# Optimization experiments

Hardware: AMD Instinct MI355X
Metric: run time of the kernel (lower is better)

The kernel has to match this reference:

```python
import jax, jax.numpy as jnp
import numpy as np

DMODEL = 1024
NHEAD = 16
HDIM = DMODEL // NHEAD
CTXLEN = 2048
BATCH = 2


def setup_inputs() -> dict:
    key = jax.random.key(0)
    k_x, k_qkv, k_pw, k_pb = jax.random.split(key, 4)
    x = jax.random.normal(k_x, (BATCH, CTXLEN, DMODEL), dtype=jnp.float32)
    # nn.Linear weights: stored as [out, in]; init scale ~ 1/sqrt(in)
    s = 1.0 / np.sqrt(DMODEL)
    w_qkv = jax.random.uniform(k_qkv, (3 * DMODEL, DMODEL), minval=-s, maxval=s, dtype=jnp.float32)
    w_proj = jax.random.uniform(k_pw, (DMODEL, DMODEL), minval=-s, maxval=s, dtype=jnp.float32)
    b_proj = jax.random.uniform(k_pb, (DMODEL,), minval=-s, maxval=s, dtype=jnp.float32)
    return {"x": x, "w_qkv": w_qkv, "w_proj": w_proj, "b_proj": b_proj}


def reference(x, w_qkv, w_proj, b_proj):
    b, t, c = x.shape
    qkv = jnp.einsum('btc,oc->bto', x, w_qkv)  # [b, t, 3c]
    q, k, v = jnp.split(qkv, 3, axis=-1)
    # [b, nhead, t, hdim]
    q = q.reshape(b, t, NHEAD, HDIM).transpose(0, 2, 1, 3)
    k = k.reshape(b, t, NHEAD, HDIM).transpose(0, 2, 1, 3)
    v = v.reshape(b, t, NHEAD, HDIM).transpose(0, 2, 1, 3)
    # NOTE: original code MULTIPLIES by sqrt(hdim) (not the usual divide)
    att = jnp.einsum('bhqd,bhkd->bhqk', q, k) * (HDIM ** 0.5)
    causal = jnp.tril(jnp.ones((t, t), dtype=bool))  # [t, t]
    att = jnp.where(causal[None, None], att, -jnp.inf)
    att = jax.nn.softmax(att, axis=-1)
    y = jnp.einsum('bhqk,bhkd->bhqd', att, v)
    y = y.transpose(0, 2, 1, 3).reshape(b, t, c)
    return jnp.einsum('btc,oc->bto', y, w_proj) + b_proj
```

## Files before the change

### kernel.cpp

```cpp
#include <hip/hip_runtime.h>
#include <hip/hip_bf16.h>

#define DMODEL 1024
#define NHEAD 16
#define HDIM 64
#define CTXLEN 2048
#define BATCH 2
#define M_TOTAL (BATCH * CTXLEN)

typedef unsigned short ushort_t;
typedef __attribute__((ext_vector_type(8))) _Float16 f16x8;
typedef __attribute__((ext_vector_type(8))) unsigned short u16x8;
typedef __attribute__((ext_vector_type(4))) float f32x4;
typedef __attribute__((ext_vector_type(4))) unsigned short u16x4;

__device__ __forceinline__ unsigned short f32_f16(float f) {
    return __builtin_bit_cast(unsigned short, (_Float16)f);
}
__device__ __forceinline__ float fast_exp2(float x) {
    return __builtin_amdgcn_exp2f(x);
}
__device__ __forceinline__ f32x4 mfma16f(f16x8 a, f16x8 b, f32x4 c) {
    return __builtin_amdgcn_mfma_f32_16x16x32_f16(a, b, c, 0, 0, 0);
}
__device__ __forceinline__ void gload_lds16(const ushort_t* g, ushort_t* l) {
    __builtin_amdgcn_global_load_lds(
        (const __attribute__((address_space(1))) void*)g,
        (__attribute__((address_space(3))) void*)l, 16, 0, 0);
}

__global__ __launch_bounds__(256)
void conv_f32_f16(const float* __restrict__ src, ushort_t* __restrict__ dst, int n4) {
    for (int i = blockIdx.x * blockDim.x + threadIdx.x; i < n4;
         i += gridDim.x * blockDim.x) {
        const float4 v = reinterpret_cast<const float4*>(src)[i];
        u16x4 o;
        o[0] = f32_f16(v.x); o[1] = f32_f16(v.y);
        o[2] = f32_f16(v.z); o[3] = f32_f16(v.w);
        reinterpret_cast<u16x4*>(dst)[i] = o;
    }
}

template<bool QKV_EPI>
__global__ __launch_bounds__(256)
void gemm_f16_nt(const ushort_t* __restrict__ A, const ushort_t* __restrict__ B,
                 const float* __restrict__ bias, float* __restrict__ C,
                 ushort_t* __restrict__ qf, ushort_t* __restrict__ kf,
                 ushort_t* __restrict__ vb,
                 int M, int N, int K) {
    __shared__ ushort_t lds[2 * 4096];

    const int tid  = threadIdx.x;
    const int lane = tid & 63;
    const int wave = tid >> 6;
    const int lc   = lane & 15;
    const int lg   = lane >> 4;
    const int wr   = wave >> 1;
    const int wc   = wave & 1;
    const int row0 = blockIdx.y * 128;
    const int col0 = blockIdx.x * 128;

    const int c0 = tid, c1 = 256 + tid;
    const int r0 = c0 >> 2, l0 = (c0 & 3) ^ ((c0 >> 3) & 3);
    const int r1 = c1 >> 2, l1 = (c1 & 3) ^ ((c1 >> 3) & 3);
    const size_t gaoff0 = (size_t)(row0 + r0) * K + l0 * 8;
    const size_t gaoff1 = (size_t)(row0 + r1) * K + l1 * 8;
    const size_t gboff0 = (size_t)(col0 + r0) * K + l0 * 8;
    const size_t gboff1 = (size_t)(col0 + r1) * K + l1 * 8;
    const int ld0 = c0 * 8, ld1 = c1 * 8;

    int aoff[4], boff[4];
    #pragma unroll
    for (int m = 0; m < 4; ++m) {
        const int ra = wr * 64 + m * 16 + lc;
        aoff[m] = ra * 32 + ((lg ^ ((ra >> 1) & 3)) * 8);
        const int rb = wc * 64 + m * 16 + lc;
        boff[m] = rb * 32 + ((lg ^ ((rb >> 1) & 3)) * 8);
    }

    f32x4 acc[4][4];
    const f32x4 zero4 = {0.f, 0.f, 0.f, 0.f};
    #pragma unroll
    for (int m = 0; m < 4; ++m)
        #pragma unroll
        for (int n = 0; n < 4; ++n) acc[m][n] = zero4;

    const int NT = K >> 5;

    auto stage = [&](int kt) {
        const int ko = kt * 32;
        gload_lds16(A + gaoff0 + ko, &lds[ld0]);
        gload_lds16(A + gaoff1 + ko, &lds[ld1]);
        gload_lds16(B + gboff0 + ko, &lds[4096 + ld0]);
        gload_lds16(B + gboff1 + ko, &lds[4096 + ld1]);
    };

    stage(0);
    for (int kt = 0; kt < NT; ++kt) {
        __syncthreads();
        f16x8 fa[4], fb[4];
        #pragma unroll
        for (int m = 0; m < 4; ++m) {
            fa[m] = *reinterpret_cast<const f16x8*>(&lds[aoff[m]]);
            fb[m] = *reinterpret_cast<const f16x8*>(&lds[4096 + boff[m]]);
        }
        __syncthreads();
        if (kt + 1 < NT) stage(kt + 1);
        #pragma unroll
        for (int m = 0; m < 4; ++m)
            #pragma unroll
            for (int n = 0; n < 4; ++n)
                acc[m][n] = mfma16f(fa[m], fb[n], acc[m][n]);
    }

    if (!QKV_EPI) {
        #pragma unroll
        for (int m = 0; m < 4; ++m)
            #pragma unroll
            for (int i = 0; i < 4; ++i) {
                const int r = row0 + wr * 64 + m * 16 + lg * 4 + i;
                #pragma unroll
                for (int n = 0; n < 4; ++n) {
                    const int c = col0 + wc * 64 + n * 16 + lc;
                    C[(size_t)r * N + c] = acc[m][n][i] + bias[c];
                }
            }
    } else {
        #pragma unroll
        for (int m = 0; m < 4; ++m)
            #pragma unroll
            for (int i = 0; i < 4; ++i) {
                const int r = row0 + wr * 64 + m * 16 + lg * 4 + i;
                const int bb = r >> 11;
                const int t  = r & 2047;
                #pragma unroll
                for (int n = 0; n < 4; ++n) {
                    const int cg  = col0 + wc * 64 + n * 16 + lc;
                    const int sec = cg >> 10;
                    const int ch  = cg & 1023;
                    const int hh  = ch >> 6;
                    const int d   = ch & 63;
                    const size_t off = (((size_t)(bb * NHEAD + hh)) * CTXLEN + t) * HDIM + d;
                    const unsigned short hv = f32_f16(acc[m][n][i]);
                    if (sec == 0)      qf[off] = hv;
                    else if (sec == 1) kf[off] = hv;
                    else               vb[off] = hv;
                }
            }
    }
}

__global__ __launch_bounds__(256)
void transpose_v(const ushort_t* __restrict__ vb, ushort_t* __restrict__ vt) {
    __shared__ ushort_t T[64][66];
    const int tt = blockIdx.x;
    const int bh = blockIdx.y;
    const int tid = threadIdx.x;
    const int r  = tid >> 2;
    const int c0 = (tid & 3) * 16;

    const ushort_t* src = vb + ((size_t)bh * CTXLEN + tt * 64) * HDIM;
    #pragma unroll
    for (int half = 0; half < 2; ++half) {
        const u16x8 v = *reinterpret_cast<const u16x8*>(&src[(size_t)r * HDIM + c0 + half * 8]);
        #pragma unroll
        for (int j = 0; j < 8; ++j) T[r][c0 + half * 8 + j] = v[j];
    }
    __syncthreads();
    ushort_t* dst = vt + ((size_t)bh * HDIM + r) * CTXLEN + tt * 64 + c0;
    u16x8 o0, o1;
    #pragma unroll
    for (int j = 0; j < 8; ++j) { o0[j] = T[c0 + j][r]; o1[j] = T[c0 + 8 + j][r]; }
    *reinterpret_cast<u16x8*>(&dst[0]) = o0;
    *reinterpret_cast<u16x8*>(&dst[8]) = o1;
}

#define SCALE_LOG2 11.5415603271f

__global__ __launch_bounds__(256)
void attn_fwd6(const ushort_t* __restrict__ qf, const ushort_t* __restrict__ kf,
               const ushort_t* __restrict__ vt, ushort_t* __restrict__ yb) {
    __shared__ ushort_t KH[2][4096];
    __shared__ ushort_t VT[2][4096];
    __shared__ ushort_t Ps[4][16][64];

    const int id   = blockIdx.x;
    const int bh   = id & 31;
    const int qraw = id >> 5;
    const int jj   = qraw >> 3, g = qraw & 7;
    const int qb   = 8 * jj + ((jj & 1) ? g : 7 - g);
    const int b    = bh >> 4;
    const int h    = bh & 15;

    const int tid  = threadIdx.x;
    const int wave = tid >> 6;
    const int lane = tid & 63;
    const int lc   = lane & 15;
    const int lg   = lane >> 4;

    const ushort_t* kfb = kf + (size_t)bh * CTXLEN * HDIM;
    const ushort_t* vtb = vt + (size_t)bh * HDIM * CTXLEN;

    const int cA = tid, cB = 256 + tid;
    const int rA = cA >> 3, sgA = (cA & 7) ^ (rA & 7);
    const int rB = cB >> 3, sgB = (cB & 7) ^ (rB & 7);

    auto stage = [&](int kb, int buf) {
        const size_t koff = (size_t)(kb * 64);
        gload_lds16(kfb + (koff + rA) * HDIM + sgA * 8, &KH[buf][cA * 8]);
        gload_lds16(kfb + (koff + rB) * HDIM + sgB * 8, &KH[buf][cB * 8]);
        gload_lds16(vtb + (size_t)rA * CTXLEN + kb * 64 + sgA * 8, &VT[buf][cA * 8]);
        gload_lds16(vtb + (size_t)rB * CTXLEN + kb * 64 + sgB * 8, &VT[buf][cB * 8]);
    };

    const size_t qrow = (size_t)bh * CTXLEN + qb * 64 + wave * 16 + lc;
    f16x8 qfr[2];
    #pragma unroll
    for (int ds = 0; ds < 2; ++ds)
        qfr[ds] = *reinterpret_cast<const f16x8*>(&qf[qrow * HDIM + ds * 32 + lg * 8]);

    const f32x4 zero4 = {0.f, 0.f, 0.f, 0.f};
    f32x4 yacc[4];
    #pragma unroll
    for (int t = 0; t < 4; ++t) yacc[t] = zero4;
    float m_i = -1e30f, l_i = 0.f;

    stage(0, 0);
    __syncthreads();

    int cur = 0;
    for (int kb = 0; kb <= qb; ++kb) {
        if (kb < qb) stage(kb + 1, cur ^ 1);

        f16x8 kfr[4][2];
        #pragma unroll
        for (int tc = 0; tc < 4; ++tc) {
            const int rk = tc * 16 + lc;
            #pragma unroll
            for (int ds = 0; ds < 2; ++ds) {
                const int a = rk * 64 + (((ds * 4 + lg) ^ (rk & 7)) * 8);
                kfr[tc][ds] = *reinterpret_cast<const f16x8*>(&KH[cur][a]);
            }
        }
        f16x8 vf[4][2];
        #pragma unroll
        for (int t = 0; t < 4; ++t) {
            const int rv = t * 16 + lc;
            #pragma unroll
            for (int ks = 0; ks < 2; ++ks) {
                const int a = rv * 64 + (((ks * 4 + lg) ^ (rv & 7)) * 8);
                vf[t][ks] = *reinterpret_cast<const f16x8*>(&VT[cur][a]);
            }
        }

        f32x4 sacc[4];
        #pragma unroll
        for (int tc = 0; tc < 4; ++tc) sacc[tc] = zero4;
        __builtin_amdgcn_s_setprio(1);
        #pragma unroll
        for (int tc = 0; tc < 4; ++tc)
            #pragma unroll
            for (int ds = 0; ds < 2; ++ds)
                sacc[tc] = mfma16f(kfr[tc][ds], qfr[ds], sacc[tc]);
        __builtin_amdgcn_s_setprio(0);

        const bool diag = (kb == qb);
        const int q_loc = wave * 16 + lc;
        float p[4][4];
        #pragma unroll
        for (int tc = 0; tc < 4; ++tc)
            #pragma unroll
            for (int i = 0; i < 4; ++i) {
                float u = sacc[tc][i] * SCALE_LOG2;
                if (diag && (tc * 16 + lg * 4 + i) > q_loc) u = -1e30f;
                p[tc][i] = u;
            }
        float mx = p[0][0];
        #pragma unroll
        for (int tc = 0; tc < 4; ++tc)
            #pragma unroll
            for (int i = 0; i < 4; ++i) mx = fmaxf(mx, p[tc][i]);
        mx = fmaxf(mx, __shfl_xor(mx, 16));
        mx = fmaxf(mx, __shfl_xor(mx, 32));
        const float mnew = fmaxf(m_i, mx);
        const float corr = fast_exp2(m_i - mnew);
        float psum = 0.f;
        #pragma unroll
        for (int tc = 0; tc < 4; ++tc)
            #pragma unroll
            for (int i = 0; i < 4; ++i) {
                const float e = fast_exp2(p[tc][i] - mnew);
                p[tc][i] = e;
                psum += e;
            }
        psum += __shfl_xor(psum, 16);
        psum += __shfl_xor(psum, 32);
        l_i = l_i * corr + psum;
        m_i = mnew;
        #pragma unroll
        for (int t = 0; t < 4; ++t) yacc[t] *= corr;

        #pragma unroll
        for (int tc = 0; tc < 4; ++tc) {
            const int eb = tc * 16 + lg * 4;
            const int se = ((((eb >> 3) ^ (lc & 7)) << 3) | (eb & 7));
            u16x4 pk;
            #pragma unroll
            for (int i = 0; i < 4; ++i) pk[i] = f32_f16(p[tc][i]);
            *reinterpret_cast<u16x4*>(&Ps[wave][lc][se]) = pk;
        }
        f16x8 pa[2];
        #pragma unroll
        for (int ks = 0; ks < 2; ++ks) {
            const int sl = ((ks * 4 + lg) ^ (lc & 7)) << 3;
            pa[ks] = *reinterpret_cast<const f16x8*>(&Ps[wave][lc][sl]);
        }
        __builtin_amdgcn_s_setprio(1);
        #pragma unroll
        for (int t = 0; t < 4; ++t)
            #pragma unroll
            for (int ks = 0; ks < 2; ++ks)
                yacc[t] = mfma16f(vf[t][ks], pa[ks], yacc[t]);
        __builtin_amdgcn_s_setprio(0);

        __syncthreads();
        cur ^= 1;
    }

    const float inv = 1.0f / l_i;
    ushort_t* base = yb + (size_t)(b * CTXLEN + qb * 64 + wave * 16 + lc) * DMODEL
                     + h * HDIM;
    #pragma unroll
    for (int t = 0; t < 4; ++t) {
        u16x4 o;
        #pragma unroll
        for (int i = 0; i < 4; ++i) o[i] = f32_f16(yacc[t][i] * inv);
        *reinterpret_cast<u16x4*>(&base[t * 16 + lg * 4]) = o;
    }
}

extern "C" void kernel_launch(void* const* d_in, const int* in_sizes, int n_in,
                              void* d_out, int out_size, void* d_ws, size_t ws_size,
                              hipStream_t stream) {
    const float* x      = (const float*)d_in[0];
    const float* w_qkv  = (const float*)d_in[1];
    const float* w_proj = (const float*)d_in[2];
    const float* b_proj = (const float*)d_in[3];
    float* out = (float*)d_out;

    char* ws = (char*)d_ws;
    ushort_t* wqf = (ushort_t*)(ws);
    ushort_t* wpf = (ushort_t*)(ws + 6291456);
    ushort_t* xf  = (ushort_t*)(ws + 8388608);
    ushort_t* qf  = (ushort_t*)(ws + 16777216);
    ushort_t* kf  = (ushort_t*)(ws + 25165824);
    ushort_t* vb  = (ushort_t*)(ws + 33554432);
    ushort_t* vt  = (ushort_t*)(ws + 41943040);
    ushort_t* yb  = xf;

    const dim3 blk(256);

    conv_f32_f16<<<dim3(2048), blk, 0, stream>>>(x, xf, M_TOTAL * DMODEL / 4);
    conv_f32_f16<<<dim3(2048), blk, 0, stream>>>(w_qkv, wqf, 3 * DMODEL * DMODEL / 4);
    conv_f32_f16<<<dim3(1024), blk, 0, stream>>>(w_proj, wpf, DMODEL * DMODEL / 4);

    gemm_f16_nt<true><<<dim3(3 * DMODEL / 128, M_TOTAL / 128), blk, 0, stream>>>(
        xf, wqf, nullptr, nullptr, qf, kf, vb, M_TOTAL, 3 * DMODEL, DMODEL);

    transpose_v<<<dim3(CTXLEN / 64, BATCH * NHEAD), blk, 0, stream>>>(vb, vt);

    attn_fwd6<<<dim3(1024), blk, 0, stream>>>(qf, kf, vt, yb);

    gemm_f16_nt<false><<<dim3(DMODEL / 128, M_TOTAL / 128), blk, 0, stream>>>(
        yb, wpf, b_proj, out, nullptr, nullptr, nullptr, M_TOTAL, DMODEL, DMODEL);
}
```

Measured before the change: 127.4 us.

## Split causal attention KV range into units with a separate merge kernel

Splits each query tile's key range into up to four units, with more units for later tiles, so the 2560 blocks do roughly equal work. Each unit writes its unnormalized partial output plus running max and sum to workspace, and a new merge kernel combines them with log-sum-exp weights before writing y. This targets load imbalance and the tail of long diagonal-heavy blocks in the causal attention. In exchange it adds an extra launch and extra global traffic for the partial results, and the partials are rounded to fp16 before normalization.

```diff
diff --git a/kernel.cpp b/kernel.cpp
--- a/kernel.cpp
+++ b/kernel.cpp
@@ -17,6 +17,9 @@
 __device__ __forceinline__ unsigned short f32_f16(float f) {
     return __builtin_bit_cast(unsigned short, (_Float16)f);
 }
+__device__ __forceinline__ float f16_f32(unsigned short h) {
+    return (float)__builtin_bit_cast(_Float16, h);
+}
 __device__ __forceinline__ float fast_exp2(float x) {
     return __builtin_amdgcn_exp2f(x);
 }
@@ -27,6 +30,12 @@
     __builtin_amdgcn_global_load_lds(
         (const __attribute__((address_space(1))) void*)g,
         (__attribute__((address_space(3))) void*)l, 16, 0, 0);
+}
+__device__ __forceinline__ int unit_off(int qt) {
+    if (qt < 8)  return qt;
+    if (qt < 16) return 8 + (qt - 8) * 2;
+    if (qt < 24) return 24 + (qt - 16) * 3;
+    return 48 + (qt - 24) * 4;
 }
 
 __global__ __launch_bounds__(256)
@@ -178,19 +187,27 @@
 #define SCALE_LOG2 11.5415603271f
 
 __global__ __launch_bounds__(256)
-void attn_fwd6(const ushort_t* __restrict__ qf, const ushort_t* __restrict__ kf,
-               const ushort_t* __restrict__ vt, ushort_t* __restrict__ yb) {
+void attn_fwd7(const ushort_t* __restrict__ qf, const ushort_t* __restrict__ kf,
+               const ushort_t* __restrict__ vt,
+               ushort_t* __restrict__ py, float* __restrict__ pml) {
     __shared__ ushort_t KH[2][4096];
     __shared__ ushort_t VT[2][4096];
     __shared__ ushort_t Ps[4][16][64];
 
-    const int id   = blockIdx.x;
-    const int bh   = id & 31;
-    const int qraw = id >> 5;
-    const int jj   = qraw >> 3, g = qraw & 7;
-    const int qb   = 8 * jj + ((jj & 1) ? g : 7 - g);
-    const int b    = bh >> 4;
-    const int h    = bh & 15;
+    const int id    = blockIdx.x;
+    const int bh    = id & 31;
+    const int u_off = id >> 5;
+    int qt, u;
+    if (u_off < 8)       { qt = u_off;                          u = 0; }
+    else if (u_off < 24) { const int t = u_off - 8;  qt = 8  + (t >> 1); u = t & 1; }
+    else if (u_off < 48) { const int t = u_off - 24; const int q3 = t / 3; qt = 16 + q3; u = t - q3 * 3; }
+    else                 { const int t = u_off - 48; qt = 24 + (t >> 2); u = t & 3; }
+    const int total = qt + 1;
+    const int nu    = (qt >> 3) + 1;
+    const int base  = total / nu, rem = total % nu;
+    const int kb0   = u * base + (u < rem ? u : rem);
+    const int len   = base + (u < rem ? 1 : 0);
+    const int slot  = bh * 80 + u_off;
 
     const int tid  = threadIdx.x;
     const int wave = tid >> 6;
@@ -213,7 +230,7 @@
         gload_lds16(vtb + (size_t)rB * CTXLEN + kb * 64 + sgB * 8, &VT[buf][cB * 8]);
     };
 
-    const size_t qrow = (size_t)bh * CTXLEN + qb * 64 + wave * 16 + lc;
+    const size_t qrow = (size_t)bh * CTXLEN + qt * 64 + wave * 16 + lc;
     f16x8 qfr[2];
     #pragma unroll
     for (int ds = 0; ds < 2; ++ds)
@@ -225,12 +242,13 @@
     for (int t = 0; t < 4; ++t) yacc[t] = zero4;
     float m_i = -1e30f, l_i = 0.f;
 
-    stage(0, 0);
+    stage(kb0, 0);
     __syncthreads();
 
     int cur = 0;
-    for (int kb = 0; kb <= qb; ++kb) {
-        if (kb < qb) stage(kb + 1, cur ^ 1);
+    for (int s = 0; s < len; ++s) {
+        const int kb = kb0 + s;
+        if (s + 1 < len) stage(kb + 1, cur ^ 1);
 
         f16x8 kfr[4][2];
         #pragma unroll
@@ -264,16 +282,16 @@
                 sacc[tc] = mfma16f(kfr[tc][ds], qfr[ds], sacc[tc]);
         __builtin_amdgcn_s_setprio(0);
 
-        const bool diag = (kb == qb);
+        const bool diag = (kb == qt);
         const int q_loc = wave * 16 + lc;
         float p[4][4];
         #pragma unroll
         for (int tc = 0; tc < 4; ++tc)
             #pragma unroll
             for (int i = 0; i < 4; ++i) {
-                float u = sacc[tc][i] * SCALE_LOG2;
-                if (diag && (tc * 16 + lg * 4 + i) > q_loc) u = -1e30f;
-                p[tc][i] = u;
+                float uu = sacc[tc][i] * SCALE_LOG2;
+                if (diag && (tc * 16 + lg * 4 + i) > q_loc) uu = -1e30f;
+                p[tc][i] = uu;
             }
         float mx = p[0][0];
         #pragma unroll
@@ -327,16 +345,79 @@
         cur ^= 1;
     }
 
-    const float inv = 1.0f / l_i;
-    ushort_t* base = yb + (size_t)(b * CTXLEN + qb * 64 + wave * 16 + lc) * DMODEL
-                     + h * HDIM;
+    const int row = wave * 16 + lc;
+    ushort_t* prow = py + ((size_t)slot * 64 + row) * 64;
     #pragma unroll
     for (int t = 0; t < 4; ++t) {
         u16x4 o;
         #pragma unroll
-        for (int i = 0; i < 4; ++i) o[i] = f32_f16(yacc[t][i] * inv);
-        *reinterpret_cast<u16x4*>(&base[t * 16 + lg * 4]) = o;
-    }
+        for (int i = 0; i < 4; ++i) o[i] = f32_f16(yacc[t][i]);
+        *reinterpret_cast<u16x4*>(&prow[t * 16 + lg * 4]) = o;
+    }
+    if (lg == 0) {
+        pml[(size_t)slot * 128 + row]      = m_i;
+        pml[(size_t)slot * 128 + 64 + row] = l_i;
+    }
+}
+
+__global__ __launch_bounds__(256)
+void merge_attn(const ushort_t* __restrict__ py, const float* __restrict__ pml,
+                ushort_t* __restrict__ yb) {
+    const int bid = blockIdx.x;
+    const int bh  = bid >> 5;
+    const int qt  = bid & 31;
+    const int b   = bh >> 4;
+    const int h   = bh & 15;
+    const int tid = threadIdx.x;
+    const int row = tid >> 2;
+    const int d0  = (tid & 3) * 16;
+
+    const int nu    = (qt >> 3) + 1;
+    const int sbase = bh * 80 + unit_off(qt);
+
+    float mu[4], lu[4];
+    float M = -1e30f;
+    #pragma unroll
+    for (int u = 0; u < 4; ++u) {
+        if (u < nu) {
+            mu[u] = pml[(size_t)(sbase + u) * 128 + row];
+            lu[u] = pml[(size_t)(sbase + u) * 128 + 64 + row];
+            M = fmaxf(M, mu[u]);
+        } else { mu[u] = -1e30f; lu[u] = 0.f; }
+    }
+    float w[4], ltot = 0.f;
+    #pragma unroll
+    for (int u = 0; u < 4; ++u) {
+        w[u] = (u < nu) ? fast_exp2(mu[u] - M) : 0.f;
+        ltot += w[u] * lu[u];
+    }
+
+    float y[16];
+    #pragma unroll
+    for (int j = 0; j < 16; ++j) y[j] = 0.f;
+    #pragma unroll
+    for (int u = 0; u < 4; ++u) {
+        if (u < nu) {
+            const ushort_t* pr = py + ((size_t)(sbase + u) * 64 + row) * 64 + d0;
+            const u16x8 a = *reinterpret_cast<const u16x8*>(&pr[0]);
+            const u16x8 c = *reinterpret_cast<const u16x8*>(&pr[8]);
+            #pragma unroll
+            for (int j = 0; j < 8; ++j) {
+                y[j]     += w[u] * f16_f32(a[j]);
+                y[8 + j] += w[u] * f16_f32(c[j]);
+            }
+        }
+    }
+    const float inv = 1.0f / ltot;
+    ushort_t* dst = yb + (size_t)(b * CTXLEN + qt * 64 + row) * DMODEL + h * HDIM + d0;
+    u16x8 o0, o1;
+    #pragma unroll
+    for (int j = 0; j < 8; ++j) {
+        o0[j] = f32_f16(y[j] * inv);
+        o1[j] = f32_f16(y[8 + j] * inv);
+    }
+    *reinterpret_cast<u16x8*>(&dst[0]) = o0;
+    *reinterpret_cast<u16x8*>(&dst[8]) = o1;
 }
 
 extern "C" void kernel_launch(void* const* d_in, const int* in_sizes, int n_in,
@@ -356,6 +437,8 @@
     ushort_t* kf  = (ushort_t*)(ws + 25165824);
     ushort_t* vb  = (ushort_t*)(ws + 33554432);
     ushort_t* vt  = (ushort_t*)(ws + 41943040);
+    ushort_t* py  = (ushort_t*)(ws + 50331648);
+    float*    pml = (float*)   (ws + 71303168);
     ushort_t* yb  = xf;
 
     const dim3 blk(256);
@@ -369,7 +452,8 @@
 
     transpose_v<<<dim3(CTXLEN / 64, BATCH * NHEAD), blk, 0, stream>>>(vb, vt);
 
-    attn_fwd6<<<dim3(1024), blk, 0, stream>>>(qf, kf, vt, yb);
+    attn_fwd7<<<dim3(2560), blk, 0, stream>>>(qf, kf, vt, py, pml);
+    merge_attn<<<dim3(1024), blk, 0, stream>>>(py, pml, yb);
 
     gemm_f16_nt<false><<<dim3(DMODEL / 128, M_TOTAL / 128), blk, 0, stream>>>(
         yb, wpf, b_proj, out, nullptr, nullptr, nullptr, M_TOTAL, DMODEL, DMODEL);
```

New measurement: 126.9 us. About the same (-0.4%).
